# Performance work log

Measured on AMD Instinct MI355X. Metric: run time of the kernel, lower is better.

Reference implementation:

```python
import jax, jax.numpy as jnp
import numpy as np

B, LQ, C = 4, 4096, 384
NH, NL, NP = 6, 1, 4
HL, WL = 64, 64
LV = HL * WL
DH = C // NH
EPS = 1e-6


def layer_norm(x, g, b):
    mu = jnp.mean(x, axis=-1, keepdims=True)
    var = jnp.mean(jnp.square(x - mu), axis=-1, keepdims=True)
    return (x - mu) * jax.lax.rsqrt(var + EPS) * g + b


def ms_deform_attn_core(value, spatial_shapes, level_start_index, loc, attn_w):
    # value [B,LV,NH,DH]; loc [B,LQ,NH,NL,NP,2] in [0,1]; attn_w [B,LQ,NH,NL,NP]
    ss = np.asarray(spatial_shapes)
    lsi = np.asarray(level_start_index)
    Bv, _, nH, dh = value.shape
    Lq = loc.shape[1]
    nP = loc.shape[4]
    out = jnp.zeros((Bv, Lq, nH, dh), value.dtype)
    for l in range(loc.shape[3]):
        Hl, Wl = int(ss[l, 0]), int(ss[l, 1])
        st = int(lsi[l])
        vflat = value[:, st:st + Hl * Wl]  # [B, Hl*Wl, nH, dh]
        xy = loc[:, :, :, l]               # [B,LQ,nH,NP,2]
        # grid_sample(align_corners=False): pixel = loc * size - 0.5
        x = xy[..., 0] * Wl - 0.5
        y = xy[..., 1] * Hl - 0.5
        x0 = jnp.floor(x)
        y0 = jnp.floor(y)
        wx = x - x0
        wy = y - y0
        x0i = x0.astype(jnp.int32)
        y0i = y0.astype(jnp.int32)

        def gather(xi, yi):
            # zero padding outside the feature map (padding_mode='zeros')
            valid = (xi >= 0) & (xi < Wl) & (yi >= 0) & (yi < Hl)
            idx = jnp.clip(yi, 0, Hl - 1) * Wl + jnp.clip(xi, 0, Wl - 1)  # [B,LQ,nH,NP]
            idx2 = idx.transpose(0, 1, 3, 2).reshape(Bv, Lq * nP, nH)
            g = jnp.take_along_axis(vflat, idx2[..., None], axis=1)       # [B,LQ*NP,nH,dh]
            g = g.reshape(Bv, Lq, nP, nH, dh).transpose(0, 1, 3, 2, 4)    # [B,LQ,nH,NP,dh]
            return g * valid[..., None].astype(value.dtype)

        samp = (gather(x0i, y0i) * ((1 - wx) * (1 - wy))[..., None]
                + gather(x0i + 1, y0i) * (wx * (1 - wy))[..., None]
                + gather(x0i, y0i + 1) * ((1 - wx) * wy)[..., None]
                + gather(x0i + 1, y0i + 1) * (wx * wy)[..., None])
        out = out + jnp.einsum('bqhpd,bqhp->bqhd', samp, attn_w[:, :, :, l])
    return out.reshape(Bv, Lq, nH * dh)


def setup_inputs() -> dict:
    key = jax.random.key(0)
    ks = jax.random.split(key, 12)
    s = 0.02
    return {
        'query': jax.random.normal(ks[0], (B, LQ, C), jnp.float32),
        'reference_points': jax.random.uniform(ks[1], (B, LQ, NL, 2), dtype=jnp.float32),
        'feat': jax.random.normal(ks[2], (B, LV, C), jnp.float32),
        'spatial_shapes': jnp.array([[HL, WL]], jnp.int32),
        'level_start_index': jnp.array([0], jnp.int32),
        'ln_q_g': jnp.ones((C,), jnp.float32), 'ln_q_b': jnp.zeros((C,), jnp.float32),
        'ln_f_g': jnp.ones((C,), jnp.float32), 'ln_f_b': jnp.zeros((C,), jnp.float32),
        'gamma': jax.random.normal(ks[3], (C,), jnp.float32) * 0.1,
        'Wv': jax.random.normal(ks[4], (C, C), jnp.float32) * s,
        'bv': jnp.zeros((C,), jnp.float32),
        'Wo': jax.random.normal(ks[5], (C, NH * NL * NP * 2), jnp.float32) * s,
        'bo': jax.random.normal(ks[6], (NH * NL * NP * 2,), jnp.float32) * 0.5,
        'Wa': jax.random.normal(ks[7], (C, NH * NL * NP), jnp.float32) * s,
        'ba': jnp.zeros((NH * NL * NP,), jnp.float32),
        'Wout': jax.random.normal(ks[8], (C, C), jnp.float32) * s,
        'bout': jnp.zeros((C,), jnp.float32),
    }


def reference(query, reference_points, feat, spatial_shapes, level_start_index,
              ln_q_g, ln_q_b, ln_f_g, ln_f_b, gamma,
              Wv, bv, Wo, bo, Wa, ba, Wout, bout):
    q = layer_norm(query, ln_q_g, ln_q_b)
    f = layer_norm(feat, ln_f_g, ln_f_b)
    value = (f @ Wv + bv).reshape(B, LV, NH, DH)
    offsets = (q @ Wo + bo).reshape(B, LQ, NH, NL, NP, 2)
    attn_w = jax.nn.softmax((q @ Wa + ba).reshape(B, LQ, NH, NL * NP), axis=-1)
    attn_w = attn_w.reshape(B, LQ, NH, NL, NP)
    # offset normalizer is (W, H) per level
    norm = jnp.stack([spatial_shapes[:, 1], spatial_shapes[:, 0]], -1).astype(jnp.float32)
    loc = reference_points[:, :, None, :, None, :] + offsets / norm[None, None, None, :, None, :]
    attn = ms_deform_attn_core(value, spatial_shapes, level_start_index, loc, attn_w)
    attn = attn @ Wout + bout
    return query + gamma * attn
```

## Files before the change

kernel.cpp:

```cpp
#include <hip/hip_runtime.h>
#include <math.h>

#define B_    4
#define LQ_   4096
#define C_    384
#define NH_   6
#define NP_   4
#define HL_   64
#define WL_   64
#define LV_   (HL_ * WL_)
#define ROWS_ (B_ * LQ_)
#define EPS_  1e-6f
#define NOFF_ 48
#define NLOG_ 24

typedef unsigned short u16;
typedef __bf16 bf16x8 __attribute__((ext_vector_type(8)));
typedef float  f32x4  __attribute__((ext_vector_type(4)));

__device__ __forceinline__ float bf2f(u16 v) {
    unsigned int u = ((unsigned int)v) << 16;
    return __uint_as_float(u);
}
__device__ __forceinline__ u16 f2bf(float f) {
    unsigned int u = __float_as_uint(f);
    u += 0x7fff + ((u >> 16) & 1);
    return (u16)(u >> 16);
}

__device__ __forceinline__ f32x4 mfma16(bf16x8 a, bf16x8 b, f32x4 c) {
    return __builtin_amdgcn_mfma_f32_16x16x32_bf16(a, b, c, 0, 0, 0);
}

__device__ __forceinline__ void gl_lds16(const u16* g, u16* l) {
    __builtin_amdgcn_global_load_lds(
        (const __attribute__((address_space(1))) unsigned int*)g,
        (__attribute__((address_space(3))) unsigned int*)l, 16, 0, 0);
}

__global__ __launch_bounds__(256) void prep_weights(
    const float* __restrict__ Wv, const float* __restrict__ Wout,
    const float* __restrict__ Wo, const float* __restrict__ Wa,
    const float* __restrict__ bo, const float* __restrict__ ba,
    u16* __restrict__ WvT, u16* __restrict__ WoutT, u16* __restrict__ WcT,
    float* __restrict__ bias_c)
{
    const int KN = 384 * 384;
    int idx = blockIdx.x * 256 + threadIdx.x;
    if (idx < KN) {
        int n = idx / 384, k = idx - n * 384;
        WvT[idx] = f2bf(Wv[k * 384 + n]);
    } else if (idx < 2 * KN) {
        int t = idx - KN;
        int n = t / 384, k = t - n * 384;
        WoutT[t] = f2bf(Wout[k * 384 + n]);
    } else if (idx < 2 * KN + 80 * 384) {
        int t = idx - 2 * KN;
        int n = t / 384, k = t - n * 384;
        float v = (n < 48) ? Wo[k * 48 + n] : (n < 72 ? Wa[k * 24 + (n - 48)] : 0.f);
        WcT[t] = f2bf(v);
    } else if (idx < 2 * KN + 80 * 384 + 80) {
        int n = idx - (2 * KN + 80 * 384);
        bias_c[n] = (n < 48) ? bo[n] : (n < 72 ? ba[n - 48] : 0.f);
    }
}

__global__ __launch_bounds__(256) void ln_kernel(
    const float* __restrict__ query, const float* __restrict__ feat,
    const float* __restrict__ qg, const float* __restrict__ qb,
    const float* __restrict__ fg, const float* __restrict__ fb,
    u16* __restrict__ qout, u16* __restrict__ fout)
{
    int wid  = threadIdx.x >> 6;
    int lane = threadIdx.x & 63;
    int row  = blockIdx.x * 4 + wid;
    const float *src, *g, *bsh;
    u16* dst;
    int r;
    if (row < ROWS_) { src = query; g = qg; bsh = qb; dst = qout; r = row; }
    else             { src = feat;  g = fg; bsh = fb; dst = fout; r = row - ROWS_; }

    const float* x = src + (size_t)r * C_;
    float v[6];
    float s = 0.f;
#pragma unroll
    for (int k = 0; k < 6; ++k) { v[k] = x[lane + 64 * k]; s += v[k]; }
#pragma unroll
    for (int off = 32; off; off >>= 1) s += __shfl_xor(s, off);
    float mu = s * (1.f / C_);

    float s2 = 0.f;
#pragma unroll
    for (int k = 0; k < 6; ++k) { float d = v[k] - mu; s2 += d * d; }
#pragma unroll
    for (int off = 32; off; off >>= 1) s2 += __shfl_xor(s2, off);
    float rs = rsqrtf(s2 * (1.f / C_) + EPS_);

    u16* y = dst + (size_t)r * C_;
#pragma unroll
    for (int k = 0; k < 6; ++k) {
        int c = lane + 64 * k;
        y[c] = f2bf((v[k] - mu) * rs * g[c] + bsh[c]);
    }
}

__global__ __launch_bounds__(256) void mfma_gemm_value(
    const u16* __restrict__ A, const u16* __restrict__ Bt,
    const float* __restrict__ bias, u16* __restrict__ Cout)
{
    const int K = 384, N = 384;
    __shared__ __align__(16) u16 As[128 * 32];
    __shared__ __align__(16) u16 Bs[128 * 32];

    int tid  = threadIdx.x;
    int lane = tid & 63, wid = tid >> 6;
    int m0 = blockIdx.y * 128, n0 = blockIdx.x * 128;
    int wm = (wid >> 1) * 64, wn = (wid & 1) * 64;
    int fr = lane & 15, quad = lane >> 4;

    int srow = tid >> 2;
    int scol = (tid & 3) * 8;
    const u16* agp0 = A  + (size_t)(m0 + srow) * K + scol;
    const u16* agp1 = A  + (size_t)(m0 + srow + 64) * K + scol;
    const u16* bgp0 = Bt + (size_t)(n0 + srow) * K + scol;
    const u16* bgp1 = Bt + (size_t)(n0 + srow + 64) * K + scol;
    u16* al0 = As + tid * 8;  u16* al1 = As + 2048 + tid * 8;
    u16* bl0 = Bs + tid * 8;  u16* bl1 = Bs + 2048 + tid * 8;

    f32x4 zero = {0.f, 0.f, 0.f, 0.f};
    f32x4 acc[4][4];
#pragma unroll
    for (int i = 0; i < 4; ++i)
#pragma unroll
        for (int j = 0; j < 4; ++j) acc[i][j] = zero;

    for (int k0 = 0; k0 < K; k0 += 32) {
        gl_lds16(agp0 + k0, al0);
        gl_lds16(agp1 + k0, al1);
        gl_lds16(bgp0 + k0, bl0);
        gl_lds16(bgp1 + k0, bl1);
        __syncthreads();
        bf16x8 af[4], bfr[4];
#pragma unroll
        for (int i = 0; i < 4; ++i)
            af[i] = *(bf16x8*)&As[(wm + i * 16 + fr) * 32 + quad * 8];
#pragma unroll
        for (int j = 0; j < 4; ++j)
            bfr[j] = *(bf16x8*)&Bs[(wn + j * 16 + fr) * 32 + quad * 8];
#pragma unroll
        for (int i = 0; i < 4; ++i)
#pragma unroll
            for (int j = 0; j < 4; ++j)
                acc[i][j] = mfma16(af[i], bfr[j], acc[i][j]);
        __syncthreads();
    }

#pragma unroll
    for (int i = 0; i < 4; ++i) {
        int row = m0 + wm + i * 16 + quad * 4;
#pragma unroll
        for (int j = 0; j < 4; ++j) {
            int col = n0 + wn + j * 16 + fr;
            float bcol = bias[col];
#pragma unroll
            for (int r = 0; r < 4; ++r) {
                float v = acc[i][j][r] + bcol;
                Cout[(size_t)(row + r) * N + col] = f2bf(v);
            }
        }
    }
}

__global__ __launch_bounds__(256) void mfma_small(
    const u16* __restrict__ A, const u16* __restrict__ Bt,
    const float* __restrict__ bias,
    float* __restrict__ offs, float* __restrict__ logits)
{
    const int K = 384;
    __shared__ __align__(16) u16 Bs[80 * 384];
    __shared__ __align__(16) u16 As[64 * 32];

    int tid  = threadIdx.x;
    int lane = tid & 63, wid = tid >> 6;
    int m0 = blockIdx.x * 64;
    int fr = lane & 15, quad = lane >> 4;

    for (int i = tid; i < 3840; i += 256)
        ((float4*)Bs)[i] = ((const float4*)Bt)[i];

    int srow = tid >> 2, scol = (tid & 3) * 8;
    const u16* agp = A + (size_t)(m0 + srow) * K + scol;
    u16* al = As + tid * 8;

    f32x4 zero = {0.f, 0.f, 0.f, 0.f};
    f32x4 acc[5];
#pragma unroll
    for (int j = 0; j < 5; ++j) acc[j] = zero;

    __syncthreads();

    for (int k0 = 0; k0 < K; k0 += 32) {
        gl_lds16(agp + k0, al);
        __syncthreads();
        bf16x8 af = *(bf16x8*)&As[(wid * 16 + fr) * 32 + quad * 8];
#pragma unroll
        for (int j = 0; j < 5; ++j) {
            bf16x8 bf = *(bf16x8*)&Bs[(j * 16 + fr) * 384 + k0 + quad * 8];
            acc[j] = mfma16(af, bf, acc[j]);
        }
        __syncthreads();
    }

    int row = m0 + wid * 16 + quad * 4;
#pragma unroll
    for (int j = 0; j < 5; ++j) {
        int col = j * 16 + fr;
        if (col < 72) {
            float bcol = bias[col];
#pragma unroll
            for (int r = 0; r < 4; ++r) {
                float v = acc[j][r] + bcol;
                if (col < 48) offs[(size_t)(row + r) * NOFF_ + col] = v;
                else          logits[(size_t)(row + r) * NLOG_ + (col - 48)] = v;
            }
        }
    }
}

#define QT_   32
#define APAD_ 392

__global__ __launch_bounds__(256) void fused_sample_out(
    const u16*  __restrict__ value,
    const float* __restrict__ rp,
    const float* __restrict__ offs,
    const float* __restrict__ logits,
    const u16*  __restrict__ WoutT,
    const float* __restrict__ bout,
    const float* __restrict__ gamma,
    const float* __restrict__ query,
    float* __restrict__ out)
{
    __shared__ float meta[QT_ * NH_ * NP_ * 4];
    __shared__ __align__(16) u16 attn_s[QT_ * APAD_];

    int t  = threadIdx.x;
    int m0 = blockIdx.x * QT_;
    int b  = m0 / LQ_;

#pragma unroll
    for (int j = 0; j < 3; ++j) {
        int u = t + 256 * j;
        int q = u / (NH_ * NP_);
        int rem = u - q * (NH_ * NP_);
        int h = rem >> 2, p = rem & 3;
        int r = m0 + q;

        const float* lg = logits + (size_t)r * NLOG_ + h * 4;
        float l0 = lg[0], l1 = lg[1], l2 = lg[2], l3 = lg[3];
        float mx = fmaxf(fmaxf(l0, l1), fmaxf(l2, l3));
        float e0 = expf(l0 - mx), e1 = expf(l1 - mx);
        float e2 = expf(l2 - mx), e3 = expf(l3 - mx);
        float den = e0 + e1 + e2 + e3;
        float ep = (p == 0) ? e0 : (p == 1) ? e1 : (p == 2) ? e2 : e3;
        float aw = ep / den;

        float rx = rp[(size_t)r * 2 + 0];
        float ry = rp[(size_t)r * 2 + 1];
        float ox = offs[(size_t)r * NOFF_ + (h * 4 + p) * 2 + 0];
        float oy = offs[(size_t)r * NOFF_ + (h * 4 + p) * 2 + 1];
        float x = rx * (float)WL_ + ox - 0.5f;
        float y = ry * (float)HL_ + oy - 0.5f;
        float x0f = floorf(x), y0f = floorf(y);
        int x0 = (int)x0f, y0 = (int)y0f;

        int midx = u * 4;
        meta[midx + 0] = x - x0f;
        meta[midx + 1] = y - y0f;
        meta[midx + 2] = aw;
        meta[midx + 3] = __int_as_float((y0 << 16) | (x0 & 0xffff));
    }
    __syncthreads();

#pragma unroll
    for (int j = 0; j < 6; ++j) {
        int v = t + 256 * j;
        int q = v / 48, dc = v - q * 48;
        int h = dc >> 3;
        int col0 = dc << 3;
        const u16* vbase = value + (size_t)b * LV_ * C_ + col0;

        float acc[8] = {0.f, 0.f, 0.f, 0.f, 0.f, 0.f, 0.f, 0.f};
#pragma unroll
        for (int p = 0; p < NP_; ++p) {
            int midx = ((q * NH_ + h) * NP_ + p) * 4;
            float wx = meta[midx + 0];
            float wy = meta[midx + 1];
            float aw = meta[midx + 2];
            int packed = __float_as_int(meta[midx + 3]);
            int x0 = (packed << 16) >> 16;
            int y0 = packed >> 16;
#pragma unroll
            for (int c = 0; c < 4; ++c) {
                int xi = x0 + (c & 1);
                int yi = y0 + (c >> 1);
                bool valid = (xi >= 0) && (xi < WL_) && (yi >= 0) && (yi < HL_);
                int xc = xi < 0 ? 0 : (xi > WL_ - 1 ? WL_ - 1 : xi);
                int yc = yi < 0 ? 0 : (yi > HL_ - 1 ? HL_ - 1 : yi);
                float w = ((c & 1) ? wx : 1.f - wx) * ((c >> 1) ? wy : 1.f - wy) * aw;
                w = valid ? w : 0.f;
                bf16x8 vv = *(const bf16x8*)(vbase + (size_t)(yc * WL_ + xc) * C_);
#pragma unroll
                for (int e = 0; e < 8; ++e) acc[e] += w * (float)vv[e];
            }
        }
        u16* dst = attn_s + q * APAD_ + col0;
#pragma unroll
        for (int e = 0; e < 8; ++e) dst[e] = f2bf(acc[e]);
    }
    __syncthreads();

    int lane = t & 63, wid = t >> 6;
    int fr = lane & 15, quad = lane >> 4;
    int wn0 = wid * 96;

    f32x4 zero = {0.f, 0.f, 0.f, 0.f};
    f32x4 acc[2][6];
#pragma unroll
    for (int i = 0; i < 2; ++i)
#pragma unroll
        for (int j = 0; j < 6; ++j) acc[i][j] = zero;

    for (int k0 = 0; k0 < 384; k0 += 32) {
        bf16x8 a0 = *(bf16x8*)&attn_s[(fr)      * APAD_ + k0 + quad * 8];
        bf16x8 a1 = *(bf16x8*)&attn_s[(16 + fr) * APAD_ + k0 + quad * 8];
#pragma unroll
        for (int nt = 0; nt < 6; ++nt) {
            bf16x8 bb = *(const bf16x8*)(WoutT + (size_t)(wn0 + nt * 16 + fr) * 384 + k0 + quad * 8);
            acc[0][nt] = mfma16(a0, bb, acc[0][nt]);
            acc[1][nt] = mfma16(a1, bb, acc[1][nt]);
        }
    }

#pragma unroll
    for (int nt = 0; nt < 6; ++nt) {
        int col = wn0 + nt * 16 + fr;
        float g = gamma[col], bc = bout[col];
#pragma unroll
        for (int mt = 0; mt < 2; ++mt) {
            int r0 = m0 + mt * 16 + quad * 4;
#pragma unroll
            for (int rr = 0; rr < 4; ++rr) {
                size_t o = (size_t)(r0 + rr) * C_ + col;
                out[o] = query[o] + g * (acc[mt][nt][rr] + bc);
            }
        }
    }
}

extern "C" void kernel_launch(void* const* d_in, const int* in_sizes, int n_in,
                              void* d_out, int out_size, void* d_ws, size_t ws_size,
                              hipStream_t stream)
{
    const float* query  = (const float*)d_in[0];
    const float* rp     = (const float*)d_in[1];
    const float* feat   = (const float*)d_in[2];
    const float* gamma  = (const float*)d_in[9];
    const float* Wv     = (const float*)d_in[10];
    const float* bv     = (const float*)d_in[11];
    const float* Wo     = (const float*)d_in[12];
    const float* bo     = (const float*)d_in[13];
    const float* Wa     = (const float*)d_in[14];
    const float* ba     = (const float*)d_in[15];
    const float* Wout   = (const float*)d_in[16];
    const float* bout   = (const float*)d_in[17];
    float* out = (float*)d_out;

    u16* wsu    = (u16*)d_ws;
    u16* qb     = wsu;
    u16* fb     = qb    + (size_t)ROWS_ * C_;
    u16* valb   = fb    + (size_t)ROWS_ * C_;
    u16* WvT    = valb  + (size_t)ROWS_ * C_;
    u16* WoutT  = WvT   + 384 * 384;
    u16* WcT    = WoutT + 384 * 384;
    float* offs   = (float*)(WcT + 80 * 384);
    float* logits = offs + (size_t)ROWS_ * NOFF_;
    float* bias_c = logits + (size_t)ROWS_ * NLOG_;

    prep_weights<<<1273, 256, 0, stream>>>(Wv, Wout, Wo, Wa, bo, ba,
                                           WvT, WoutT, WcT, bias_c);

    ln_kernel<<<8192, 256, 0, stream>>>(query, feat,
        (const float*)d_in[5], (const float*)d_in[6],
        (const float*)d_in[7], (const float*)d_in[8], qb, fb);

    mfma_gemm_value<<<dim3(3, 128), 256, 0, stream>>>(fb, WvT, bv, valb);

    mfma_small<<<256, 256, 0, stream>>>(qb, WcT, bias_c, offs, logits);

    fused_sample_out<<<ROWS_ / QT_, 256, 0, stream>>>(
        valb, rp, offs, logits, WoutT, bout, gamma, query, out);
}
```

Baseline: 190.6 us.

## Merge launches, retile GEMMs, shrink sampling tile with batch-interleaved block order

Merges the layernorm and weight-prep kernels into one launch. Also merges the value-projection GEMM and the offset/logit GEMM into one launch, with retiled value blocks (128x64) and a 128-row tile for the small GEMM. The fused sample+output kernel now handles 16 queries per block with 512 threads. Block IDs are interleaved across batches, likely to spread value-map accesses over the cache. Together these cut launch count and raise block count and occupancy, at the cost of less reuse of Wout per block in the output projection.

```diff
diff --git a/kernel.cpp b/kernel.cpp
--- a/kernel.cpp
+++ b/kernel.cpp
@@ -38,199 +38,205 @@
         (__attribute__((address_space(3))) unsigned int*)l, 16, 0, 0);
 }
 
-__global__ __launch_bounds__(256) void prep_weights(
+#define LN_BLOCKS_   8192
+#define PREP_BLOCKS_ 1273
+
+__global__ __launch_bounds__(256) void ln_prep(
+    const float* __restrict__ query, const float* __restrict__ feat,
+    const float* __restrict__ qg, const float* __restrict__ qbv,
+    const float* __restrict__ fg, const float* __restrict__ fbv,
+    u16* __restrict__ qout, u16* __restrict__ fout,
     const float* __restrict__ Wv, const float* __restrict__ Wout,
     const float* __restrict__ Wo, const float* __restrict__ Wa,
     const float* __restrict__ bo, const float* __restrict__ ba,
     u16* __restrict__ WvT, u16* __restrict__ WoutT, u16* __restrict__ WcT,
     float* __restrict__ bias_c)
 {
-    const int KN = 384 * 384;
-    int idx = blockIdx.x * 256 + threadIdx.x;
-    if (idx < KN) {
-        int n = idx / 384, k = idx - n * 384;
-        WvT[idx] = f2bf(Wv[k * 384 + n]);
-    } else if (idx < 2 * KN) {
-        int t = idx - KN;
-        int n = t / 384, k = t - n * 384;
-        WoutT[t] = f2bf(Wout[k * 384 + n]);
-    } else if (idx < 2 * KN + 80 * 384) {
-        int t = idx - 2 * KN;
-        int n = t / 384, k = t - n * 384;
-        float v = (n < 48) ? Wo[k * 48 + n] : (n < 72 ? Wa[k * 24 + (n - 48)] : 0.f);
-        WcT[t] = f2bf(v);
-    } else if (idx < 2 * KN + 80 * 384 + 80) {
-        int n = idx - (2 * KN + 80 * 384);
-        bias_c[n] = (n < 48) ? bo[n] : (n < 72 ? ba[n - 48] : 0.f);
-    }
-}
-
-__global__ __launch_bounds__(256) void ln_kernel(
-    const float* __restrict__ query, const float* __restrict__ feat,
-    const float* __restrict__ qg, const float* __restrict__ qb,
-    const float* __restrict__ fg, const float* __restrict__ fb,
-    u16* __restrict__ qout, u16* __restrict__ fout)
+    if (blockIdx.x < LN_BLOCKS_) {
+        int wid  = threadIdx.x >> 6;
+        int lane = threadIdx.x & 63;
+        int row  = blockIdx.x * 4 + wid;
+        const float *src, *g, *bsh;
+        u16* dst;
+        int r;
+        if (row < ROWS_) { src = query; g = qg; bsh = qbv; dst = qout; r = row; }
+        else             { src = feat;  g = fg; bsh = fbv; dst = fout; r = row - ROWS_; }
+
+        const float* x = src + (size_t)r * C_;
+        float v[6];
+        float s = 0.f;
+#pragma unroll
+        for (int k = 0; k < 6; ++k) { v[k] = x[lane + 64 * k]; s += v[k]; }
+#pragma unroll
+        for (int off = 32; off; off >>= 1) s += __shfl_xor(s, off);
+        float mu = s * (1.f / C_);
+
+        float s2 = 0.f;
+#pragma unroll
+        for (int k = 0; k < 6; ++k) { float d = v[k] - mu; s2 += d * d; }
+#pragma unroll
+        for (int off = 32; off; off >>= 1) s2 += __shfl_xor(s2, off);
+        float rs = rsqrtf(s2 * (1.f / C_) + EPS_);
+
+        u16* y = dst + (size_t)r * C_;
+#pragma unroll
+        for (int k = 0; k < 6; ++k) {
+            int c = lane + 64 * k;
+            y[c] = f2bf((v[k] - mu) * rs * g[c] + bsh[c]);
+        }
+    } else {
+        const int KN = 384 * 384;
+        int idx = (blockIdx.x - LN_BLOCKS_) * 256 + threadIdx.x;
+        if (idx < KN) {
+            int n = idx / 384, k = idx - n * 384;
+            WvT[idx] = f2bf(Wv[k * 384 + n]);
+        } else if (idx < 2 * KN) {
+            int t = idx - KN;
+            int n = t / 384, k = t - n * 384;
+            WoutT[t] = f2bf(Wout[k * 384 + n]);
+        } else if (idx < 2 * KN + 80 * 384) {
+            int t = idx - 2 * KN;
+            int n = t / 384, k = t - n * 384;
+            float v = (n < 48) ? Wo[k * 48 + n] : (n < 72 ? Wa[k * 24 + (n - 48)] : 0.f);
+            WcT[t] = f2bf(v);
+        } else if (idx < 2 * KN + 80 * 384 + 80) {
+            int n = idx - (2 * KN + 80 * 384);
+            bias_c[n] = (n < 48) ? bo[n] : (n < 72 ? ba[n - 48] : 0.f);
+        }
+    }
+}
+
+__global__ __launch_bounds__(256) void gemm_combined(
+    const u16* __restrict__ fb, const u16* __restrict__ qb,
+    const u16* __restrict__ WvT, const u16* __restrict__ WcT,
+    const float* __restrict__ bv, const float* __restrict__ bias_c,
+    u16* __restrict__ valb, float* __restrict__ offs, float* __restrict__ logits)
 {
-    int wid  = threadIdx.x >> 6;
-    int lane = threadIdx.x & 63;
-    int row  = blockIdx.x * 4 + wid;
-    const float *src, *g, *bsh;
-    u16* dst;
-    int r;
-    if (row < ROWS_) { src = query; g = qg; bsh = qb; dst = qout; r = row; }
-    else             { src = feat;  g = fg; bsh = fb; dst = fout; r = row - ROWS_; }
-
-    const float* x = src + (size_t)r * C_;
-    float v[6];
-    float s = 0.f;
-#pragma unroll
-    for (int k = 0; k < 6; ++k) { v[k] = x[lane + 64 * k]; s += v[k]; }
-#pragma unroll
-    for (int off = 32; off; off >>= 1) s += __shfl_xor(s, off);
-    float mu = s * (1.f / C_);
-
-    float s2 = 0.f;
-#pragma unroll
-    for (int k = 0; k < 6; ++k) { float d = v[k] - mu; s2 += d * d; }
-#pragma unroll
-    for (int off = 32; off; off >>= 1) s2 += __shfl_xor(s2, off);
-    float rs = rsqrtf(s2 * (1.f / C_) + EPS_);
-
-    u16* y = dst + (size_t)r * C_;
-#pragma unroll
-    for (int k = 0; k < 6; ++k) {
-        int c = lane + 64 * k;
-        y[c] = f2bf((v[k] - mu) * rs * g[c] + bsh[c]);
-    }
-}
-
-__global__ __launch_bounds__(256) void mfma_gemm_value(
-    const u16* __restrict__ A, const u16* __restrict__ Bt,
-    const float* __restrict__ bias, u16* __restrict__ Cout)
-{
-    const int K = 384, N = 384;
+    const int K = 384;
     __shared__ __align__(16) u16 As[128 * 32];
-    __shared__ __align__(16) u16 Bs[128 * 32];
-
+    __shared__ __align__(16) u16 Bs[80 * 32];
+
+    int g    = blockIdx.x;
     int tid  = threadIdx.x;
     int lane = tid & 63, wid = tid >> 6;
-    int m0 = blockIdx.y * 128, n0 = blockIdx.x * 128;
-    int wm = (wid >> 1) * 64, wn = (wid & 1) * 64;
     int fr = lane & 15, quad = lane >> 4;
 
     int srow = tid >> 2;
     int scol = (tid & 3) * 8;
-    const u16* agp0 = A  + (size_t)(m0 + srow) * K + scol;
-    const u16* agp1 = A  + (size_t)(m0 + srow + 64) * K + scol;
-    const u16* bgp0 = Bt + (size_t)(n0 + srow) * K + scol;
-    const u16* bgp1 = Bt + (size_t)(n0 + srow + 64) * K + scol;
-    u16* al0 = As + tid * 8;  u16* al1 = As + 2048 + tid * 8;
-    u16* bl0 = Bs + tid * 8;  u16* bl1 = Bs + 2048 + tid * 8;
-
-    f32x4 zero = {0.f, 0.f, 0.f, 0.f};
-    f32x4 acc[4][4];
-#pragma unroll
-    for (int i = 0; i < 4; ++i)
-#pragma unroll
-        for (int j = 0; j < 4; ++j) acc[i][j] = zero;
-
-    for (int k0 = 0; k0 < K; k0 += 32) {
-        gl_lds16(agp0 + k0, al0);
-        gl_lds16(agp1 + k0, al1);
-        gl_lds16(bgp0 + k0, bl0);
-        gl_lds16(bgp1 + k0, bl1);
-        __syncthreads();
-        bf16x8 af[4], bfr[4];
+
+    if (g < 768) {
+        int m0 = (g / 6) * 128, n0 = (g % 6) * 64;
+        const u16* agp0 = fb  + (size_t)(m0 + srow) * K + scol;
+        const u16* agp1 = fb  + (size_t)(m0 + 64 + srow) * K + scol;
+        const u16* bgp  = WvT + (size_t)(n0 + srow) * K + scol;
+        u16* al0 = As + tid * 8;  u16* al1 = As + 2048 + tid * 8;
+        u16* bl  = Bs + tid * 8;
+
+        int wm = (wid >> 1) * 64, wn = (wid & 1) * 32;
+
+        f32x4 zero = {0.f, 0.f, 0.f, 0.f};
+        f32x4 acc[4][2];
 #pragma unroll
         for (int i = 0; i < 4; ++i)
-            af[i] = *(bf16x8*)&As[(wm + i * 16 + fr) * 32 + quad * 8];
-#pragma unroll
-        for (int j = 0; j < 4; ++j)
-            bfr[j] = *(bf16x8*)&Bs[(wn + j * 16 + fr) * 32 + quad * 8];
-#pragma unroll
-        for (int i = 0; i < 4; ++i)
-#pragma unroll
-            for (int j = 0; j < 4; ++j)
-                acc[i][j] = mfma16(af[i], bfr[j], acc[i][j]);
-        __syncthreads();
-    }
-
-#pragma unroll
-    for (int i = 0; i < 4; ++i) {
-        int row = m0 + wm + i * 16 + quad * 4;
-#pragma unroll
-        for (int j = 0; j < 4; ++j) {
-            int col = n0 + wn + j * 16 + fr;
-            float bcol = bias[col];
-#pragma unroll
-            for (int r = 0; r < 4; ++r) {
-                float v = acc[i][j][r] + bcol;
-                Cout[(size_t)(row + r) * N + col] = f2bf(v);
+#pragma unroll
+            for (int j = 0; j < 2; ++j) acc[i][j] = zero;
+
+        for (int k0 = 0; k0 < K; k0 += 32) {
+            gl_lds16(agp0 + k0, al0);
+            gl_lds16(agp1 + k0, al1);
+            gl_lds16(bgp  + k0, bl);
+            __syncthreads();
+            bf16x8 af[4], bfr[2];
+#pragma unroll
+            for (int i = 0; i < 4; ++i)
+                af[i] = *(bf16x8*)&As[(wm + i * 16 + fr) * 32 + quad * 8];
+#pragma unroll
+            for (int j = 0; j < 2; ++j)
+                bfr[j] = *(bf16x8*)&Bs[(wn + j * 16 + fr) * 32 + quad * 8];
+#pragma unroll
+            for (int i = 0; i < 4; ++i)
+#pragma unroll
+                for (int j = 0; j < 2; ++j)
+                    acc[i][j] = mfma16(af[i], bfr[j], acc[i][j]);
+            __syncthreads();
+        }
+
+#pragma unroll
+        for (int i = 0; i < 4; ++i) {
+            int row = m0 + wm + i * 16 + quad * 4;
+#pragma unroll
+            for (int j = 0; j < 2; ++j) {
+                int col = n0 + wn + j * 16 + fr;
+                float bcol = bv[col];
+#pragma unroll
+                for (int r = 0; r < 4; ++r)
+                    valb[(size_t)(row + r) * C_ + col] = f2bf(acc[i][j][r] + bcol);
             }
         }
-    }
-}
-
-__global__ __launch_bounds__(256) void mfma_small(
-    const u16* __restrict__ A, const u16* __restrict__ Bt,
-    const float* __restrict__ bias,
-    float* __restrict__ offs, float* __restrict__ logits)
-{
-    const int K = 384;
-    __shared__ __align__(16) u16 Bs[80 * 384];
-    __shared__ __align__(16) u16 As[64 * 32];
-
-    int tid  = threadIdx.x;
-    int lane = tid & 63, wid = tid >> 6;
-    int m0 = blockIdx.x * 64;
-    int fr = lane & 15, quad = lane >> 4;
-
-    for (int i = tid; i < 3840; i += 256)
-        ((float4*)Bs)[i] = ((const float4*)Bt)[i];
-
-    int srow = tid >> 2, scol = (tid & 3) * 8;
-    const u16* agp = A + (size_t)(m0 + srow) * K + scol;
-    u16* al = As + tid * 8;
-
-    f32x4 zero = {0.f, 0.f, 0.f, 0.f};
-    f32x4 acc[5];
-#pragma unroll
-    for (int j = 0; j < 5; ++j) acc[j] = zero;
-
-    __syncthreads();
-
-    for (int k0 = 0; k0 < K; k0 += 32) {
-        gl_lds16(agp + k0, al);
-        __syncthreads();
-        bf16x8 af = *(bf16x8*)&As[(wid * 16 + fr) * 32 + quad * 8];
-#pragma unroll
-        for (int j = 0; j < 5; ++j) {
-            bf16x8 bf = *(bf16x8*)&Bs[(j * 16 + fr) * 384 + k0 + quad * 8];
-            acc[j] = mfma16(af, bf, acc[j]);
-        }
-        __syncthreads();
-    }
-
-    int row = m0 + wid * 16 + quad * 4;
-#pragma unroll
-    for (int j = 0; j < 5; ++j) {
-        int col = j * 16 + fr;
-        if (col < 72) {
-            float bcol = bias[col];
-#pragma unroll
-            for (int r = 0; r < 4; ++r) {
-                float v = acc[j][r] + bcol;
-                if (col < 48) offs[(size_t)(row + r) * NOFF_ + col] = v;
-                else          logits[(size_t)(row + r) * NLOG_ + (col - 48)] = v;
+    } else {
+        int m0 = (g - 768) * 128;
+        const u16* agp0 = qb + (size_t)(m0 + srow) * K + scol;
+        const u16* agp1 = qb + (size_t)(m0 + 64 + srow) * K + scol;
+        u16* al0 = As + tid * 8;  u16* al1 = As + 2048 + tid * 8;
+        const u16* bgp0 = WcT + (size_t)srow * K + scol;
+        const u16* bgp1 = WcT + (size_t)(64 + srow) * K + scol;
+        u16* bl0 = Bs + tid * 8;
+        u16* bl1 = Bs + 2048 + tid * 8;
+
+        int wm = wid * 32;
+
+        f32x4 zero = {0.f, 0.f, 0.f, 0.f};
+        f32x4 acc[2][5];
+#pragma unroll
+        for (int i = 0; i < 2; ++i)
+#pragma unroll
+            for (int j = 0; j < 5; ++j) acc[i][j] = zero;
+
+        for (int k0 = 0; k0 < K; k0 += 32) {
+            gl_lds16(agp0 + k0, al0);
+            gl_lds16(agp1 + k0, al1);
+            gl_lds16(bgp0 + k0, bl0);
+            if (tid < 64) gl_lds16(bgp1 + k0, bl1);
+            __syncthreads();
+            bf16x8 af[2], bfr[5];
+#pragma unroll
+            for (int i = 0; i < 2; ++i)
+                af[i] = *(bf16x8*)&As[(wm + i * 16 + fr) * 32 + quad * 8];
+#pragma unroll
+            for (int j = 0; j < 5; ++j)
+                bfr[j] = *(bf16x8*)&Bs[(j * 16 + fr) * 32 + quad * 8];
+#pragma unroll
+            for (int i = 0; i < 2; ++i)
+#pragma unroll
+                for (int j = 0; j < 5; ++j)
+                    acc[i][j] = mfma16(af[i], bfr[j], acc[i][j]);
+            __syncthreads();
+        }
+
+#pragma unroll
+        for (int i = 0; i < 2; ++i) {
+            int row = m0 + wm + i * 16 + quad * 4;
+#pragma unroll
+            for (int j = 0; j < 5; ++j) {
+                int col = j * 16 + fr;
+                if (col < 72) {
+                    float bcol = bias_c[col];
+#pragma unroll
+                    for (int r = 0; r < 4; ++r) {
+                        float v = acc[i][j][r] + bcol;
+                        if (col < 48) offs[(size_t)(row + r) * NOFF_ + col] = v;
+                        else          logits[(size_t)(row + r) * NLOG_ + (col - 48)] = v;
+                    }
+                }
             }
         }
     }
 }
 
-#define QT_   32
+#define QT_   16
 #define APAD_ 392
 
-__global__ __launch_bounds__(256) void fused_sample_out(
+__global__ __launch_bounds__(512) void fused_sample_out(
     const u16*  __restrict__ value,
     const float* __restrict__ rp,
     const float* __restrict__ offs,
@@ -244,15 +250,15 @@
     __shared__ float meta[QT_ * NH_ * NP_ * 4];
     __shared__ __align__(16) u16 attn_s[QT_ * APAD_];
 
-    int t  = threadIdx.x;
-    int m0 = blockIdx.x * QT_;
-    int b  = m0 / LQ_;
-
-#pragma unroll
-    for (int j = 0; j < 3; ++j) {
-        int u = t + 256 * j;
-        int q = u / (NH_ * NP_);
-        int rem = u - q * (NH_ * NP_);
+    int t = threadIdx.x;
+    int g = blockIdx.x;
+    int b     = (g & 7) >> 1;
+    int local = ((g >> 3) << 1) | (g & 1);
+    int m0 = b * LQ_ + local * QT_;
+
+    if (t < QT_ * NH_ * NP_) {
+        int q = t / (NH_ * NP_);
+        int rem = t - q * (NH_ * NP_);
         int h = rem >> 2, p = rem & 3;
         int r = m0 + q;
 
@@ -274,7 +280,7 @@
         float x0f = floorf(x), y0f = floorf(y);
         int x0 = (int)x0f, y0 = (int)y0f;
 
-        int midx = u * 4;
+        int midx = t * 4;
         meta[midx + 0] = x - x0f;
         meta[midx + 1] = y - y0f;
         meta[midx + 2] = aw;
@@ -283,77 +289,71 @@
     __syncthreads();
 
 #pragma unroll
-    for (int j = 0; j < 6; ++j) {
-        int v = t + 256 * j;
-        int q = v / 48, dc = v - q * 48;
-        int h = dc >> 3;
-        int col0 = dc << 3;
-        const u16* vbase = value + (size_t)b * LV_ * C_ + col0;
-
-        float acc[8] = {0.f, 0.f, 0.f, 0.f, 0.f, 0.f, 0.f, 0.f};
-#pragma unroll
-        for (int p = 0; p < NP_; ++p) {
-            int midx = ((q * NH_ + h) * NP_ + p) * 4;
-            float wx = meta[midx + 0];
-            float wy = meta[midx + 1];
-            float aw = meta[midx + 2];
-            int packed = __float_as_int(meta[midx + 3]);
-            int x0 = (packed << 16) >> 16;
-            int y0 = packed >> 16;
-#pragma unroll
-            for (int c = 0; c < 4; ++c) {
-                int xi = x0 + (c & 1);
-                int yi = y0 + (c >> 1);
-                bool valid = (xi >= 0) && (xi < WL_) && (yi >= 0) && (yi < HL_);
-                int xc = xi < 0 ? 0 : (xi > WL_ - 1 ? WL_ - 1 : xi);
-                int yc = yi < 0 ? 0 : (yi > HL_ - 1 ? HL_ - 1 : yi);
-                float w = ((c & 1) ? wx : 1.f - wx) * ((c >> 1) ? wy : 1.f - wy) * aw;
-                w = valid ? w : 0.f;
-                bf16x8 vv = *(const bf16x8*)(vbase + (size_t)(yc * WL_ + xc) * C_);
-#pragma unroll
-                for (int e = 0; e < 8; ++e) acc[e] += w * (float)vv[e];
+    for (int j = 0; j < 2; ++j) {
+        int v = t + 512 * j;
+        if (v < QT_ * 48) {
+            int q = v / 48, dc = v - q * 48;
+            int h = dc >> 3;
+            int col0 = dc << 3;
+            const u16* vbase = value + (size_t)b * LV_ * C_ + col0;
+
+            float acc[8] = {0.f, 0.f, 0.f, 0.f, 0.f, 0.f, 0.f, 0.f};
+#pragma unroll
+            for (int p = 0; p < NP_; ++p) {
+                int midx = ((q * NH_ + h) * NP_ + p) * 4;
+                float wx = meta[midx + 0];
+                float wy = meta[midx + 1];
+                float aw = meta[midx + 2];
+                int packed = __float_as_int(meta[midx + 3]);
+                int x0 = (packed << 16) >> 16;
+                int y0 = packed >> 16;
+#pragma unroll
+                for (int c = 0; c < 4; ++c) {
+                    int xi = x0 + (c & 1);
+                    int yi = y0 + (c >> 1);
+                    bool valid = (xi >= 0) && (xi < WL_) && (yi >= 0) && (yi < HL_);
+                    int xc = xi < 0 ? 0 : (xi > WL_ - 1 ? WL_ - 1 : xi);
+                    int yc = yi < 0 ? 0 : (yi > HL_ - 1 ? HL_ - 1 : yi);
+                    float w = ((c & 1) ? wx : 1.f - wx) * ((c >> 1) ? wy : 1.f - wy) * aw;
+                    w = valid ? w : 0.f;
+                    bf16x8 vv = *(const bf16x8*)(vbase + (size_t)(yc * WL_ + xc) * C_);
+#pragma unroll
+                    for (int e = 0; e < 8; ++e) acc[e] += w * (float)vv[e];
+                }
             }
-        }
-        u16* dst = attn_s + q * APAD_ + col0;
-#pragma unroll
-        for (int e = 0; e < 8; ++e) dst[e] = f2bf(acc[e]);
+            u16* dst = attn_s + q * APAD_ + col0;
+#pragma unroll
+            for (int e = 0; e < 8; ++e) dst[e] = f2bf(acc[e]);
+        }
     }
     __syncthreads();
 
     int lane = t & 63, wid = t >> 6;
     int fr = lane & 15, quad = lane >> 4;
-    int wn0 = wid * 96;
+    int wn0 = wid * 48;
 
     f32x4 zero = {0.f, 0.f, 0.f, 0.f};
-    f32x4 acc[2][6];
-#pragma unroll
-    for (int i = 0; i < 2; ++i)
-#pragma unroll
-        for (int j = 0; j < 6; ++j) acc[i][j] = zero;
+    f32x4 acc[3];
+#pragma unroll
+    for (int j = 0; j < 3; ++j) acc[j] = zero;
 
     for (int k0 = 0; k0 < 384; k0 += 32) {
-        bf16x8 a0 = *(bf16x8*)&attn_s[(fr)      * APAD_ + k0 + quad * 8];
-        bf16x8 a1 = *(bf16x8*)&attn_s[(16 + fr) * APAD_ + k0 + quad * 8];
-#pragma unroll
-        for (int nt = 0; nt < 6; ++nt) {
+        bf16x8 a0 = *(bf16x8*)&attn_s[fr * APAD_ + k0 + quad * 8];
+#pragma unroll
+        for (int nt = 0; nt < 3; ++nt) {
             bf16x8 bb = *(const bf16x8*)(WoutT + (size_t)(wn0 + nt * 16 + fr) * 384 + k0 + quad * 8);
-            acc[0][nt] = mfma16(a0, bb, acc[0][nt]);
-            acc[1][nt] = mfma16(a1, bb, acc[1][nt]);
-        }
-    }
-
-#pragma unroll
-    for (int nt = 0; nt < 6; ++nt) {
+            acc[nt] = mfma16(a0, bb, acc[nt]);
+        }
+    }
+
+#pragma unroll
+    for (int nt = 0; nt < 3; ++nt) {
         int col = wn0 + nt * 16 + fr;
-        float g = gamma[col], bc = bout[col];
-#pragma unroll
-        for (int mt = 0; mt < 2; ++mt) {
-            int r0 = m0 + mt * 16 + quad * 4;
-#pragma unroll
-            for (int rr = 0; rr < 4; ++rr) {
-                size_t o = (size_t)(r0 + rr) * C_ + col;
-                out[o] = query[o] + g * (acc[mt][nt][rr] + bc);
-            }
+        float gm = gamma[col], bc = bout[col];
+#pragma unroll
+        for (int rr = 0; rr < 4; ++rr) {
+            size_t o = (size_t)(m0 + quad * 4 + rr) * C_ + col;
+            out[o] = query[o] + gm * (acc[nt][rr] + bc);
         }
     }
 }
@@ -387,17 +387,15 @@
     float* logits = offs + (size_t)ROWS_ * NOFF_;
     float* bias_c = logits + (size_t)ROWS_ * NLOG_;
 
-    prep_weights<<<1273, 256, 0, stream>>>(Wv, Wout, Wo, Wa, bo, ba,
-                                           WvT, WoutT, WcT, bias_c);
-
-    ln_kernel<<<8192, 256, 0, stream>>>(query, feat,
+    ln_prep<<<LN_BLOCKS_ + PREP_BLOCKS_, 256, 0, stream>>>(
+        query, feat,
         (const float*)d_in[5], (const float*)d_in[6],
-        (const float*)d_in[7], (const float*)d_in[8], qb, fb);
-
-    mfma_gemm_value<<<dim3(3, 128), 256, 0, stream>>>(fb, WvT, bv, valb);
-
-    mfma_small<<<256, 256, 0, stream>>>(qb, WcT, bias_c, offs, logits);
-
-    fused_sample_out<<<ROWS_ / QT_, 256, 0, stream>>>(
+        (const float*)d_in[7], (const float*)d_in[8],
+        qb, fb, Wv, Wout, Wo, Wa, bo, ba, WvT, WoutT, WcT, bias_c);
+
+    gemm_combined<<<896, 256, 0, stream>>>(fb, qb, WvT, WcT, bv, bias_c,
+                                           valb, offs, logits);
+
+    fused_sample_out<<<ROWS_ / QT_, 512, 0, stream>>>(
         valb, rp, offs, logits, WoutT, bout, gamma, query, out);
 }
```

New measurement: 191.5 us. No clear change (+0.5%).
